# Kernel tuning notes

Hardware: AMD Instinct MI355X
Metric: run time of the kernel (lower is better)

## Reference

```python
import jax, jax.numpy as jnp
import numpy as np

N, L, D_MODEL, N_HEADS = 2, 2048, 512, 8

def setup_inputs() -> dict:
    key = jax.random.key(0)
    x = jax.random.normal(key, (N, L, D_MODEL), dtype=jnp.float32)
    return {"input_data": x}

def reference(input_data):
    n, l, _ = input_data.shape
    h = N_HEADS
    d = D_MODEL // h  # head dim
    # Q = K = V = reshaped input (the Linear projections are unused in the original forward)
    q = input_data.reshape(n, l, h, d)
    k = q
    v = q
    scale = 1.0 / jnp.sqrt(jnp.float32(d))
    # scores: [n, h, l, s]
    scores = jnp.einsum('nlhd,nshd->nhls', q, k)
    attn_weights = jax.nn.softmax(scale * scores, axis=-1)
    # updated values: [n, l, h, d]
    updated_v = jnp.einsum('nhls,nshd->nlhd', attn_weights, v)
    out = updated_v.reshape(n, l, h * d)
    # attn returned as mean over heads: permute nhls -> nlhs, mean over h -> [n, l, s]
    attn = jnp.transpose(attn_weights, (0, 2, 1, 3)).mean(axis=-2)
    return (out, attn)
```

## Files before the change

kernel.cpp:

```cpp
#include <hip/hip_runtime.h>

#define NBATCH 2
#define SEQ    2048
#define DMODEL 512
#define NH     8
#define HDIM   64
#define SCALE  0.125f

typedef __attribute__((ext_vector_type(8))) short bf16x8;
typedef __attribute__((ext_vector_type(4))) float f32x4;

__device__ __forceinline__ unsigned short f2bf(float f) {
    union { float f; unsigned u; } v; v.f = f;
    unsigned r = v.u + 0x7FFFu + ((v.u >> 16) & 1u);
    return (unsigned short)(r >> 16);
}

__device__ __forceinline__ void pack4(unsigned short* dst, float4 v) {
    unsigned long long pk = (unsigned long long)f2bf(v.x)
        | ((unsigned long long)f2bf(v.y) << 16)
        | ((unsigned long long)f2bf(v.z) << 32)
        | ((unsigned long long)f2bf(v.w) << 48);
    *(unsigned long long*)dst = pk;
}

__device__ __forceinline__ bf16x8 pack8(float4 a, float4 b) {
    bf16x8 r;
    r[0]=(short)f2bf(a.x); r[1]=(short)f2bf(a.y); r[2]=(short)f2bf(a.z); r[3]=(short)f2bf(a.w);
    r[4]=(short)f2bf(b.x); r[5]=(short)f2bf(b.y); r[6]=(short)f2bf(b.z); r[7]=(short)f2bf(b.w);
    return r;
}

__device__ __forceinline__ void gld_lds16(const unsigned short* g, unsigned short* l) {
    __builtin_amdgcn_global_load_lds(
        (const __attribute__((address_space(1))) unsigned int*)(const void*)g,
        (__attribute__((address_space(3))) unsigned int*)(void*)l, 16, 0, 0);
}

__global__ __launch_bounds__(256) void prep_kernel(const float* __restrict__ x,
                                                   unsigned short* __restrict__ xb,
                                                   unsigned short* __restrict__ xt) {
    __shared__ unsigned short Tb[64][72];
    const int bid = blockIdx.x;
    const int n = bid >> 8, h = (bid >> 5) & 7, st = bid & 31;
    const int s0 = st * 64;
    const int t = threadIdx.x;
    {
        const int s = t >> 2, d0 = (t & 3) * 16;
        const float* xp = x + ((size_t)(n*SEQ + s0 + s))*DMODEL + h*HDIM + d0;
        #pragma unroll
        for (int i = 0; i < 4; ++i) pack4(&Tb[s][d0 + 4*i], *(const float4*)(xp + 4*i));
    }
    __syncthreads();
    {
        const int s = t >> 2, d0 = (t & 3) * 16;
        unsigned short* bp = xb + ((size_t)(n*SEQ + s0 + s))*DMODEL + h*HDIM + d0;
        *(bf16x8*)bp       = *(const bf16x8*)&Tb[s][d0];
        *(bf16x8*)(bp + 8) = *(const bf16x8*)&Tb[s][d0 + 8];
    }
    {
        const int d = t >> 2, c0 = (t & 3) * 16;
        bf16x8 v0, v1;
        #pragma unroll
        for (int j = 0; j < 8; ++j) {
            v0[j] = (short)Tb[c0 + j][d];
            v1[j] = (short)Tb[c0 + 8 + j][d];
        }
        unsigned short* tp = xt + ((size_t)((n*NH + h)*HDIM + d))*SEQ + s0 + c0;
        *(bf16x8*)tp       = v0;
        *(bf16x8*)(tp + 8) = v1;
    }
}

__global__ __launch_bounds__(256) void out_kernel2(const unsigned short* __restrict__ xb,
                                                   const unsigned short* __restrict__ xt,
                                                   float* __restrict__ out,
                                                   float* __restrict__ rho) {
    __shared__ unsigned short Kb[128*64];
    __shared__ unsigned short Vt[64*128];
    __shared__ unsigned short pb[64][136];

    const int bid = blockIdx.x;
    const int n = bid >> 8, h = (bid >> 5) & 7, lt = bid & 31;
    const int l0 = lt * 64;
    const int tid = threadIdx.x;
    const int wv = tid >> 6, lane = tid & 63;
    const int lr = lane & 15, lg = lane >> 4;

    const unsigned short* qp = xb + ((size_t)(n*SEQ + l0 + wv*16 + lr))*DMODEL + h*HDIM + lg*8;
    const bf16x8 a0 = *(const bf16x8*)qp;
    const bf16x8 a1 = *(const bf16x8*)(qp + 32);

    f32x4 ov0 = {0.f,0.f,0.f,0.f}, ov1 = {0.f,0.f,0.f,0.f};
    f32x4 ov2 = {0.f,0.f,0.f,0.f}, ov3 = {0.f,0.f,0.f,0.f};
    float rs[4] = {0.f,0.f,0.f,0.f};

    for (int s0 = 0; s0 < SEQ; s0 += 128) {
        __syncthreads();
        #pragma unroll
        for (int it = 0; it < 4; ++it) {
            const int row = it*32 + wv*8 + (lane >> 3);
            const int gc  = (lane & 7) ^ (row & 7);
            gld_lds16(xb + ((size_t)(n*SEQ + s0 + row))*DMODEL + h*HDIM + gc*8,
                      Kb + it*2048 + wv*512);
        }
        #pragma unroll
        for (int it = 0; it < 4; ++it) {
            const int d  = it*16 + wv*4 + (lane >> 4);
            const int gc = (lane & 15) ^ (d & 15);
            gld_lds16(xt + ((size_t)((n*NH + h)*HDIM + d))*SEQ + s0 + gc*8,
                      Vt + it*2048 + wv*512);
        }
        __syncthreads();
        #pragma unroll
        for (int ct = 0; ct < 8; ++ct) {
            const int krow = ct*16 + lr;
            const int c0 = (lg ^ (lr & 7)) << 3;
            bf16x8 b0 = *(const bf16x8*)&Kb[krow*64 + c0];
            bf16x8 b1 = *(const bf16x8*)&Kb[krow*64 + (c0 ^ 32)];
            f32x4 acc = {0.f,0.f,0.f,0.f};
            acc = __builtin_amdgcn_mfma_f32_16x16x32_bf16(a0, b0, acc, 0,0,0);
            acc = __builtin_amdgcn_mfma_f32_16x16x32_bf16(a1, b1, acc, 0,0,0);
            #pragma unroll
            for (int r = 0; r < 4; ++r) {
                const float e = __expf(acc[r] * SCALE);
                rs[r] += e;
                pb[wv*16 + lg*4 + r][ct*16 + lr] = f2bf(e);
            }
        }
        __syncthreads();
        #pragma unroll
        for (int ks = 0; ks < 4; ++ks) {
            const bf16x8 pa = *(const bf16x8*)&pb[wv*16 + lr][ks*32 + lg*8];
            const int cc = ((ks*4 + lg) ^ lr) << 3;
            const bf16x8 w0 = *(const bf16x8*)&Vt[( 0 + lr)*128 + cc];
            const bf16x8 w1 = *(const bf16x8*)&Vt[(16 + lr)*128 + cc];
            const bf16x8 w2 = *(const bf16x8*)&Vt[(32 + lr)*128 + cc];
            const bf16x8 w3 = *(const bf16x8*)&Vt[(48 + lr)*128 + cc];
            ov0 = __builtin_amdgcn_mfma_f32_16x16x32_bf16(pa, w0, ov0, 0,0,0);
            ov1 = __builtin_amdgcn_mfma_f32_16x16x32_bf16(pa, w1, ov1, 0,0,0);
            ov2 = __builtin_amdgcn_mfma_f32_16x16x32_bf16(pa, w2, ov2, 0,0,0);
            ov3 = __builtin_amdgcn_mfma_f32_16x16x32_bf16(pa, w3, ov3, 0,0,0);
        }
    }

    #pragma unroll
    for (int r = 0; r < 4; ++r) {
        float s = rs[r];
        s += __shfl_xor(s, 1, 16);
        s += __shfl_xor(s, 2, 16);
        s += __shfl_xor(s, 4, 16);
        s += __shfl_xor(s, 8, 16);
        rs[r] = s;
    }
    const int row0 = l0 + wv*16 + lg*4;
    if (lr == 0) {
        #pragma unroll
        for (int r = 0; r < 4; ++r)
            rho[(size_t)(n*NH + h)*SEQ + row0 + r] = rs[r];
    }
    #pragma unroll
    for (int r = 0; r < 4; ++r) {
        const float iv = 1.f / rs[r];
        float* op = out + ((size_t)(n*SEQ + row0 + r))*DMODEL + h*HDIM + lr;
        op[0]  = ov0[r] * iv;
        op[16] = ov1[r] * iv;
        op[32] = ov2[r] * iv;
        op[48] = ov3[r] * iv;
    }
}

__global__ __launch_bounds__(256) void mean_kernel2(const unsigned short* __restrict__ xb,
                                                    const float* __restrict__ rho,
                                                    float* __restrict__ attn) {
    __shared__ unsigned short Qb[64*64];
    __shared__ unsigned short Kb2[64*64];
    __shared__ float invb[64];

    const int bid = blockIdx.x;
    const int n = bid >> 10, lt = (bid >> 5) & 31, st = bid & 31;
    const int l0 = lt * 64, s0 = st * 64;
    const int tid = threadIdx.x;
    const int wv = tid >> 6, lane = tid & 63;
    const int lr = lane & 15, lg = lane >> 4;

    float mean[4][4];
    #pragma unroll
    for (int ct = 0; ct < 4; ++ct)
        #pragma unroll
        for (int r = 0; r < 4; ++r) mean[ct][r] = 0.f;

    for (int h = 0; h < NH; ++h) {
        __syncthreads();
        #pragma unroll
        for (int it = 0; it < 2; ++it) {
            const int row = it*32 + wv*8 + (lane >> 3);
            const int gc  = (lane & 7) ^ (row & 7);
            gld_lds16(xb + ((size_t)(n*SEQ + l0 + row))*DMODEL + h*HDIM + gc*8,
                      Qb + it*2048 + wv*512);
        }
        #pragma unroll
        for (int it = 0; it < 2; ++it) {
            const int row = it*32 + wv*8 + (lane >> 3);
            const int gc  = (lane & 7) ^ (row & 7);
            gld_lds16(xb + ((size_t)(n*SEQ + s0 + row))*DMODEL + h*HDIM + gc*8,
                      Kb2 + it*2048 + wv*512);
        }
        if (tid < 64)
            invb[tid] = 0.125f / rho[(size_t)(n*NH + h)*SEQ + l0 + tid];
        __syncthreads();

        const int qrow = wv*16 + lr;
        const int qc0 = (lg ^ (lr & 7)) << 3;
        const bf16x8 a0 = *(const bf16x8*)&Qb[qrow*64 + qc0];
        const bf16x8 a1 = *(const bf16x8*)&Qb[qrow*64 + (qc0 ^ 32)];
        #pragma unroll
        for (int ct = 0; ct < 4; ++ct) {
            const int krow = ct*16 + lr;
            const int c0 = (lg ^ (lr & 7)) << 3;
            bf16x8 b0 = *(const bf16x8*)&Kb2[krow*64 + c0];
            bf16x8 b1 = *(const bf16x8*)&Kb2[krow*64 + (c0 ^ 32)];
            f32x4 acc = {0.f,0.f,0.f,0.f};
            acc = __builtin_amdgcn_mfma_f32_16x16x32_bf16(a0, b0, acc, 0,0,0);
            acc = __builtin_amdgcn_mfma_f32_16x16x32_bf16(a1, b1, acc, 0,0,0);
            #pragma unroll
            for (int r = 0; r < 4; ++r)
                mean[ct][r] += __expf(acc[r] * SCALE) * invb[wv*16 + lg*4 + r];
        }
    }

    #pragma unroll
    for (int ct = 0; ct < 4; ++ct)
        #pragma unroll
        for (int r = 0; r < 4; ++r)
            attn[((size_t)(n*SEQ + l0 + wv*16 + lg*4 + r))*SEQ + s0 + ct*16 + lr]
                = mean[ct][r];
}

__global__ __launch_bounds__(256) void fb_out_kernel(const float* __restrict__ x,
                                                     float* __restrict__ out,
                                                     float* __restrict__ rho) {
    __shared__ unsigned short Kbuf[128][72];
    __shared__ unsigned short vT[64][136];
    __shared__ unsigned short pbuf[64][136];
    const int bid = blockIdx.x;
    const int n  = bid >> 8, h = (bid >> 5) & 7, lt = bid & 31;
    const int l0 = lt * 64;
    const int tid = threadIdx.x;
    const int wv  = tid >> 6, lane = tid & 63;
    const int lr  = lane & 15, lg = lane >> 4;
    const float* qp = x + ((size_t)(n*SEQ + l0 + wv*16 + lr))*DMODEL + h*HDIM + lg*8;
    const bf16x8 a0 = pack8(*(const float4*)qp,      *(const float4*)(qp+4));
    const bf16x8 a1 = pack8(*(const float4*)(qp+32), *(const float4*)(qp+36));
    f32x4 ov0 = {0.f,0.f,0.f,0.f}, ov1 = {0.f,0.f,0.f,0.f};
    f32x4 ov2 = {0.f,0.f,0.f,0.f}, ov3 = {0.f,0.f,0.f,0.f};
    float rs[4] = {0.f,0.f,0.f,0.f};
    for (int s0 = 0; s0 < SEQ; s0 += 128) {
        __syncthreads();
        {
            const int srow = tid >> 1, dbase = (tid & 1) * 32;
            const float* kp = x + ((size_t)(n*SEQ + s0 + srow))*DMODEL + h*HDIM + dbase;
            #pragma unroll
            for (int i = 0; i < 8; ++i) {
                float4 v = *(const float4*)(kp + 4*i);
                pack4(&Kbuf[srow][dbase + 4*i], v);
                const int d = dbase + 4*i;
                vT[d+0][srow] = f2bf(v.x); vT[d+1][srow] = f2bf(v.y);
                vT[d+2][srow] = f2bf(v.z); vT[d+3][srow] = f2bf(v.w);
            }
        }
        __syncthreads();
        #pragma unroll
        for (int ct = 0; ct < 8; ++ct) {
            const unsigned short* bp = &Kbuf[ct*16 + lr][lg*8];
            bf16x8 b0 = *(const bf16x8*)bp;
            bf16x8 b1 = *(const bf16x8*)(bp + 32);
            f32x4 acc = {0.f,0.f,0.f,0.f};
            acc = __builtin_amdgcn_mfma_f32_16x16x32_bf16(a0, b0, acc, 0,0,0);
            acc = __builtin_amdgcn_mfma_f32_16x16x32_bf16(a1, b1, acc, 0,0,0);
            #pragma unroll
            for (int r = 0; r < 4; ++r) {
                const float e = __expf(acc[r] * SCALE);
                rs[r] += e;
                pbuf[wv*16 + lg*4 + r][ct*16 + lr] = f2bf(e);
            }
        }
        __syncthreads();
        #pragma unroll
        for (int ks = 0; ks < 4; ++ks) {
            bf16x8 pa = *(const bf16x8*)&pbuf[wv*16 + lr][ks*32 + lg*8];
            bf16x8 v0 = *(const bf16x8*)&vT[ 0 + lr][ks*32 + lg*8];
            bf16x8 v1 = *(const bf16x8*)&vT[16 + lr][ks*32 + lg*8];
            bf16x8 v2 = *(const bf16x8*)&vT[32 + lr][ks*32 + lg*8];
            bf16x8 v3 = *(const bf16x8*)&vT[48 + lr][ks*32 + lg*8];
            ov0 = __builtin_amdgcn_mfma_f32_16x16x32_bf16(pa, v0, ov0, 0,0,0);
            ov1 = __builtin_amdgcn_mfma_f32_16x16x32_bf16(pa, v1, ov1, 0,0,0);
            ov2 = __builtin_amdgcn_mfma_f32_16x16x32_bf16(pa, v2, ov2, 0,0,0);
            ov3 = __builtin_amdgcn_mfma_f32_16x16x32_bf16(pa, v3, ov3, 0,0,0);
        }
    }
    #pragma unroll
    for (int r = 0; r < 4; ++r) {
        float s = rs[r];
        s += __shfl_xor(s, 1, 16); s += __shfl_xor(s, 2, 16);
        s += __shfl_xor(s, 4, 16); s += __shfl_xor(s, 8, 16);
        rs[r] = s;
    }
    const int row0 = l0 + wv*16 + lg*4;
    if (lr == 0) {
        #pragma unroll
        for (int r = 0; r < 4; ++r)
            rho[(size_t)(n*NH + h)*SEQ + row0 + r] = rs[r];
    }
    #pragma unroll
    for (int r = 0; r < 4; ++r) {
        const float iv = 1.f / rs[r];
        float* op = out + ((size_t)(n*SEQ + row0 + r))*DMODEL + h*HDIM + lr;
        op[0] = ov0[r]*iv; op[16] = ov1[r]*iv; op[32] = ov2[r]*iv; op[48] = ov3[r]*iv;
    }
}

__global__ __launch_bounds__(256) void fb_mean_kernel(const float* __restrict__ x,
                                                      const float* __restrict__ rho,
                                                      float* __restrict__ attn) {
    __shared__ unsigned short Qb[64][72];
    __shared__ unsigned short Kb[128][72];
    __shared__ float          invb[64];
    const int bid = blockIdx.x;
    const int n  = bid >> 9, lt = (bid >> 4) & 31, st = bid & 15;
    const int l0 = lt * 64, s0 = st * 128;
    const int tid = threadIdx.x;
    const int wv  = tid >> 6, lane = tid & 63;
    const int lr  = lane & 15, lg = lane >> 4;
    float mean[8][4];
    #pragma unroll
    for (int ct = 0; ct < 8; ++ct)
        #pragma unroll
        for (int r = 0; r < 4; ++r) mean[ct][r] = 0.f;
    for (int h = 0; h < NH; ++h) {
        __syncthreads();
        {
            const int qrow = tid >> 2, qd = (tid & 3) * 16;
            const float* qp = x + ((size_t)(n*SEQ + l0 + qrow))*DMODEL + h*HDIM + qd;
            #pragma unroll
            for (int i = 0; i < 4; ++i)
                pack4(&Qb[qrow][qd + 4*i], *(const float4*)(qp + 4*i));
        }
        {
            const int srow = tid >> 1, dbase = (tid & 1) * 32;
            const float* kp = x + ((size_t)(n*SEQ + s0 + srow))*DMODEL + h*HDIM + dbase;
            #pragma unroll
            for (int i = 0; i < 8; ++i)
                pack4(&Kb[srow][dbase + 4*i], *(const float4*)(kp + 4*i));
        }
        if (tid < 64)
            invb[tid] = 0.125f / rho[(size_t)(n*NH + h)*SEQ + l0 + tid];
        __syncthreads();
        const unsigned short* ap = &Qb[wv*16 + lr][lg*8];
        const bf16x8 a0 = *(const bf16x8*)ap;
        const bf16x8 a1 = *(const bf16x8*)(ap + 32);
        #pragma unroll
        for (int ct = 0; ct < 8; ++ct) {
            const unsigned short* bp = &Kb[ct*16 + lr][lg*8];
            bf16x8 b0 = *(const bf16x8*)bp;
            bf16x8 b1 = *(const bf16x8*)(bp + 32);
            f32x4 acc = {0.f,0.f,0.f,0.f};
            acc = __builtin_amdgcn_mfma_f32_16x16x32_bf16(a0, b0, acc, 0,0,0);
            acc = __builtin_amdgcn_mfma_f32_16x16x32_bf16(a1, b1, acc, 0,0,0);
            #pragma unroll
            for (int r = 0; r < 4; ++r)
                mean[ct][r] += __expf(acc[r] * SCALE) * invb[wv*16 + lg*4 + r];
        }
    }
    #pragma unroll
    for (int ct = 0; ct < 8; ++ct)
        #pragma unroll
        for (int r = 0; r < 4; ++r)
            attn[((size_t)(n*SEQ + l0 + wv*16 + lg*4 + r))*SEQ + s0 + ct*16 + lr]
                = mean[ct][r];
}

extern "C" void kernel_launch(void* const* d_in, const int* in_sizes, int n_in,
                              void* d_out, int out_size, void* d_ws, size_t ws_size,
                              hipStream_t stream) {
    (void)in_sizes; (void)n_in; (void)out_size;
    const float* x = (const float*)d_in[0];
    float* out  = (float*)d_out;
    float* attn = out + (size_t)NBATCH*SEQ*DMODEL;
    float* rho  = (float*)d_ws;

    const size_t XB_OFF = 131072;
    const size_t XT_OFF = XB_OFF + 4194304;
    const size_t NEED   = XT_OFF + 4194304;

    if (ws_size >= NEED) {
        unsigned short* xb = (unsigned short*)((char*)d_ws + XB_OFF);
        unsigned short* xt = (unsigned short*)((char*)d_ws + XT_OFF);
        prep_kernel <<<dim3(512),  dim3(256), 0, stream>>>(x, xb, xt);
        out_kernel2 <<<dim3(512),  dim3(256), 0, stream>>>(xb, xt, out, rho);
        mean_kernel2<<<dim3(2048), dim3(256), 0, stream>>>(xb, rho, attn);
    } else {
        fb_out_kernel <<<dim3(512),  dim3(256), 0, stream>>>(x, out, rho);
        fb_mean_kernel<<<dim3(1024), dim3(256), 0, stream>>>(x, rho, attn);
    }
}
```

Before: 85.03 us.

## Double-buffer K/V and Q/K LDS tiles and remap block order across XCDs

Both attention kernels now double-buffer their LDS tiles. The next K/V chunk, or the next head's Q/K tiles, is issued before the current one is computed, so each iteration needs only one barrier instead of two. The output kernel shrinks its key chunk from 128 to 64 to fit the two buffers. The mean kernel preloads the inverse row sums for all heads up front. Block indices are permuted so that neighbouring work lands on the same XCD, aiming for better L2 reuse; the trade-off is more loop iterations and reliance on the async global-to-LDS loads completing before the end-of-iteration barrier.

```diff
diff --git a/kernel.cpp b/kernel.cpp
--- a/kernel.cpp
+++ b/kernel.cpp
@@ -72,15 +72,16 @@
     }
 }
 
-__global__ __launch_bounds__(256) void out_kernel2(const unsigned short* __restrict__ xb,
+__global__ __launch_bounds__(256) void out_kernel3(const unsigned short* __restrict__ xb,
                                                    const unsigned short* __restrict__ xt,
                                                    float* __restrict__ out,
                                                    float* __restrict__ rho) {
-    __shared__ unsigned short Kb[128*64];
-    __shared__ unsigned short Vt[64*128];
-    __shared__ unsigned short pb[64][136];
-
-    const int bid = blockIdx.x;
+    __shared__ unsigned short Kb[2][64*64];
+    __shared__ unsigned short Vt[2][64*64];
+    __shared__ unsigned short pb[64][72];
+
+    const int i   = blockIdx.x;
+    const int bid = (i & 7) * 64 + (i >> 3);
     const int n = bid >> 8, h = (bid >> 5) & 7, lt = bid & 31;
     const int l0 = lt * 64;
     const int tid = threadIdx.x;
@@ -91,33 +92,45 @@
     const bf16x8 a0 = *(const bf16x8*)qp;
     const bf16x8 a1 = *(const bf16x8*)(qp + 32);
 
+    const int srow8  = wv*8 + (lane >> 3);
+    const int schunk = lane & 7;
+    const unsigned short* kbase = xb + (size_t)(n*SEQ)*DMODEL + h*HDIM;
+    const unsigned short* vbase = xt + ((size_t)(n*NH + h)*HDIM)*SEQ;
+
+    auto stage = [&](int buf, int s0) {
+        #pragma unroll
+        for (int it = 0; it < 2; ++it) {
+            const int row = it*32 + srow8;
+            const int gc  = schunk ^ (row & 7);
+            gld_lds16(kbase + (size_t)(s0 + row)*DMODEL + gc*8,
+                      &Kb[buf][it*2048 + wv*512]);
+        }
+        #pragma unroll
+        for (int it = 0; it < 2; ++it) {
+            const int d  = it*32 + srow8;
+            const int gc = schunk ^ (d & 7);
+            gld_lds16(vbase + (size_t)d*SEQ + s0 + gc*8,
+                      &Vt[buf][it*2048 + wv*512]);
+        }
+    };
+
     f32x4 ov0 = {0.f,0.f,0.f,0.f}, ov1 = {0.f,0.f,0.f,0.f};
     f32x4 ov2 = {0.f,0.f,0.f,0.f}, ov3 = {0.f,0.f,0.f,0.f};
     float rs[4] = {0.f,0.f,0.f,0.f};
 
-    for (int s0 = 0; s0 < SEQ; s0 += 128) {
-        __syncthreads();
-        #pragma unroll
-        for (int it = 0; it < 4; ++it) {
-            const int row = it*32 + wv*8 + (lane >> 3);
-            const int gc  = (lane & 7) ^ (row & 7);
-            gld_lds16(xb + ((size_t)(n*SEQ + s0 + row))*DMODEL + h*HDIM + gc*8,
-                      Kb + it*2048 + wv*512);
-        }
-        #pragma unroll
-        for (int it = 0; it < 4; ++it) {
-            const int d  = it*16 + wv*4 + (lane >> 4);
-            const int gc = (lane & 15) ^ (d & 15);
-            gld_lds16(xt + ((size_t)((n*NH + h)*HDIM + d))*SEQ + s0 + gc*8,
-                      Vt + it*2048 + wv*512);
-        }
-        __syncthreads();
-        #pragma unroll
-        for (int ct = 0; ct < 8; ++ct) {
-            const int krow = ct*16 + lr;
-            const int c0 = (lg ^ (lr & 7)) << 3;
-            bf16x8 b0 = *(const bf16x8*)&Kb[krow*64 + c0];
-            bf16x8 b1 = *(const bf16x8*)&Kb[krow*64 + (c0 ^ 32)];
+    stage(0, 0);
+    __syncthreads();
+    int cur = 0;
+
+    for (int c = 0; c < 32; ++c) {
+        if (c < 31) stage(cur ^ 1, (c + 1) * 64);
+
+        const int c0 = (lg ^ (lr & 7)) << 3;
+        #pragma unroll
+        for (int ct = 0; ct < 4; ++ct) {
+            const unsigned short* kr = &Kb[cur][(ct*16 + lr)*64];
+            bf16x8 b0 = *(const bf16x8*)&kr[c0];
+            bf16x8 b1 = *(const bf16x8*)&kr[c0 ^ 32];
             f32x4 acc = {0.f,0.f,0.f,0.f};
             acc = __builtin_amdgcn_mfma_f32_16x16x32_bf16(a0, b0, acc, 0,0,0);
             acc = __builtin_amdgcn_mfma_f32_16x16x32_bf16(a1, b1, acc, 0,0,0);
@@ -128,20 +141,21 @@
                 pb[wv*16 + lg*4 + r][ct*16 + lr] = f2bf(e);
             }
         }
-        __syncthreads();
-        #pragma unroll
-        for (int ks = 0; ks < 4; ++ks) {
+        #pragma unroll
+        for (int ks = 0; ks < 2; ++ks) {
             const bf16x8 pa = *(const bf16x8*)&pb[wv*16 + lr][ks*32 + lg*8];
-            const int cc = ((ks*4 + lg) ^ lr) << 3;
-            const bf16x8 w0 = *(const bf16x8*)&Vt[( 0 + lr)*128 + cc];
-            const bf16x8 w1 = *(const bf16x8*)&Vt[(16 + lr)*128 + cc];
-            const bf16x8 w2 = *(const bf16x8*)&Vt[(32 + lr)*128 + cc];
-            const bf16x8 w3 = *(const bf16x8*)&Vt[(48 + lr)*128 + cc];
+            const int cc = ((ks*4 + lg) ^ (lr & 7)) << 3;
+            const bf16x8 w0 = *(const bf16x8*)&Vt[cur][( 0 + lr)*64 + cc];
+            const bf16x8 w1 = *(const bf16x8*)&Vt[cur][(16 + lr)*64 + cc];
+            const bf16x8 w2 = *(const bf16x8*)&Vt[cur][(32 + lr)*64 + cc];
+            const bf16x8 w3 = *(const bf16x8*)&Vt[cur][(48 + lr)*64 + cc];
             ov0 = __builtin_amdgcn_mfma_f32_16x16x32_bf16(pa, w0, ov0, 0,0,0);
             ov1 = __builtin_amdgcn_mfma_f32_16x16x32_bf16(pa, w1, ov1, 0,0,0);
             ov2 = __builtin_amdgcn_mfma_f32_16x16x32_bf16(pa, w2, ov2, 0,0,0);
             ov3 = __builtin_amdgcn_mfma_f32_16x16x32_bf16(pa, w3, ov3, 0,0,0);
         }
+        __syncthreads();
+        cur ^= 1;
     }
 
     #pragma unroll
@@ -170,63 +184,77 @@
     }
 }
 
-__global__ __launch_bounds__(256) void mean_kernel2(const unsigned short* __restrict__ xb,
+__global__ __launch_bounds__(256) void mean_kernel3(const unsigned short* __restrict__ xb,
                                                     const float* __restrict__ rho,
                                                     float* __restrict__ attn) {
-    __shared__ unsigned short Qb[64*64];
-    __shared__ unsigned short Kb2[64*64];
-    __shared__ float invb[64];
-
-    const int bid = blockIdx.x;
+    __shared__ unsigned short Qb[2][64*64];
+    __shared__ unsigned short Kb[2][64*64];
+    __shared__ float invb[NH][64];
+
+    const int i   = blockIdx.x;
+    const int bid = (i & 7) * 256 + (i >> 3);
     const int n = bid >> 10, lt = (bid >> 5) & 31, st = bid & 31;
     const int l0 = lt * 64, s0 = st * 64;
     const int tid = threadIdx.x;
     const int wv = tid >> 6, lane = tid & 63;
     const int lr = lane & 15, lg = lane >> 4;
 
+    for (int j = tid; j < NH*64; j += 256) {
+        const int hh = j >> 6, row = j & 63;
+        invb[hh][row] = 0.125f / rho[(size_t)(n*NH + hh)*SEQ + l0 + row];
+    }
+
+    const int srow8  = wv*8 + (lane >> 3);
+    const int schunk = lane & 7;
+
+    auto stage = [&](int buf, int h) {
+        #pragma unroll
+        for (int it = 0; it < 2; ++it) {
+            const int row = it*32 + srow8;
+            const int gc  = schunk ^ (row & 7);
+            gld_lds16(xb + ((size_t)(n*SEQ + l0 + row))*DMODEL + h*HDIM + gc*8,
+                      &Qb[buf][it*2048 + wv*512]);
+        }
+        #pragma unroll
+        for (int it = 0; it < 2; ++it) {
+            const int row = it*32 + srow8;
+            const int gc  = schunk ^ (row & 7);
+            gld_lds16(xb + ((size_t)(n*SEQ + s0 + row))*DMODEL + h*HDIM + gc*8,
+                      &Kb[buf][it*2048 + wv*512]);
+        }
+    };
+
     float mean[4][4];
     #pragma unroll
     for (int ct = 0; ct < 4; ++ct)
         #pragma unroll
         for (int r = 0; r < 4; ++r) mean[ct][r] = 0.f;
 
+    stage(0, 0);
+    __syncthreads();
+    int cur = 0;
+
     for (int h = 0; h < NH; ++h) {
-        __syncthreads();
-        #pragma unroll
-        for (int it = 0; it < 2; ++it) {
-            const int row = it*32 + wv*8 + (lane >> 3);
-            const int gc  = (lane & 7) ^ (row & 7);
-            gld_lds16(xb + ((size_t)(n*SEQ + l0 + row))*DMODEL + h*HDIM + gc*8,
-                      Qb + it*2048 + wv*512);
-        }
-        #pragma unroll
-        for (int it = 0; it < 2; ++it) {
-            const int row = it*32 + wv*8 + (lane >> 3);
-            const int gc  = (lane & 7) ^ (row & 7);
-            gld_lds16(xb + ((size_t)(n*SEQ + s0 + row))*DMODEL + h*HDIM + gc*8,
-                      Kb2 + it*2048 + wv*512);
-        }
-        if (tid < 64)
-            invb[tid] = 0.125f / rho[(size_t)(n*NH + h)*SEQ + l0 + tid];
-        __syncthreads();
+        if (h < NH-1) stage(cur ^ 1, h + 1);
 
         const int qrow = wv*16 + lr;
-        const int qc0 = (lg ^ (lr & 7)) << 3;
-        const bf16x8 a0 = *(const bf16x8*)&Qb[qrow*64 + qc0];
-        const bf16x8 a1 = *(const bf16x8*)&Qb[qrow*64 + (qc0 ^ 32)];
+        const int c0 = (lg ^ (lr & 7)) << 3;
+        const bf16x8 a0 = *(const bf16x8*)&Qb[cur][qrow*64 + c0];
+        const bf16x8 a1 = *(const bf16x8*)&Qb[cur][qrow*64 + (c0 ^ 32)];
         #pragma unroll
         for (int ct = 0; ct < 4; ++ct) {
-            const int krow = ct*16 + lr;
-            const int c0 = (lg ^ (lr & 7)) << 3;
-            bf16x8 b0 = *(const bf16x8*)&Kb2[krow*64 + c0];
-            bf16x8 b1 = *(const bf16x8*)&Kb2[krow*64 + (c0 ^ 32)];
+            const unsigned short* kr = &Kb[cur][(ct*16 + lr)*64];
+            bf16x8 b0 = *(const bf16x8*)&kr[c0];
+            bf16x8 b1 = *(const bf16x8*)&kr[c0 ^ 32];
             f32x4 acc = {0.f,0.f,0.f,0.f};
             acc = __builtin_amdgcn_mfma_f32_16x16x32_bf16(a0, b0, acc, 0,0,0);
             acc = __builtin_amdgcn_mfma_f32_16x16x32_bf16(a1, b1, acc, 0,0,0);
             #pragma unroll
             for (int r = 0; r < 4; ++r)
-                mean[ct][r] += __expf(acc[r] * SCALE) * invb[wv*16 + lg*4 + r];
-        }
+                mean[ct][r] += __expf(acc[r] * SCALE) * invb[h][wv*16 + lg*4 + r];
+        }
+        __syncthreads();
+        cur ^= 1;
     }
 
     #pragma unroll
@@ -397,8 +425,8 @@
         unsigned short* xb = (unsigned short*)((char*)d_ws + XB_OFF);
         unsigned short* xt = (unsigned short*)((char*)d_ws + XT_OFF);
         prep_kernel <<<dim3(512),  dim3(256), 0, stream>>>(x, xb, xt);
-        out_kernel2 <<<dim3(512),  dim3(256), 0, stream>>>(xb, xt, out, rho);
-        mean_kernel2<<<dim3(2048), dim3(256), 0, stream>>>(xb, rho, attn);
+        out_kernel3 <<<dim3(512),  dim3(256), 0, stream>>>(xb, xt, out, rho);
+        mean_kernel3<<<dim3(2048), dim3(256), 0, stream>>>(xb, rho, attn);
     } else {
         fb_out_kernel <<<dim3(512),  dim3(256), 0, stream>>>(x, out, rho);
         fb_mean_kernel<<<dim3(1024), dim3(256), 0, stream>>>(x, rho, attn);
```

Result: slower. 89.56 us (+5.3%).
